# Kernel tuning notes

Hardware: AMD Instinct MI355X
Metric: run time of the kernel (lower is better)

## Reference

```python
import jax, jax.numpy as jnp
import numpy as np

IOU_THRESHOLD = 0.7


def _pairwise_iou(boxes):
    # boxes: [N, 4] as (y1, x1, y2, x2). Returns [N, N] IoU matrix.
    y1, x1, y2, x2 = boxes[:, 0], boxes[:, 1], boxes[:, 2], boxes[:, 3]
    area = (y2 - y1) * (x2 - x1)  # [N]
    iy1 = jnp.maximum(y1[:, None], y1[None, :])
    ix1 = jnp.maximum(x1[:, None], x1[None, :])
    iy2 = jnp.minimum(y2[:, None], y2[None, :])
    ix2 = jnp.minimum(x2[:, None], x2[None, :])
    ih = jnp.clip(iy2 - iy1, 0.0)
    iw = jnp.clip(ix2 - ix1, 0.0)
    inter = ih * iw
    union = area[:, None] + area[None, :] - inter
    return inter / jnp.maximum(union, 1e-9)


def setup_inputs() -> dict:
    key = jax.random.key(0)
    k1, k2, k3 = jax.random.split(key, 3)
    n = 8192
    img = 1024.0
    # Valid boxes: top-left corner + positive width/height, clipped to image.
    tl = jax.random.uniform(k1, (n, 2), dtype=jnp.float32) * (img - 64.0)
    wh = 16.0 + jax.random.uniform(k2, (n, 2), dtype=jnp.float32) * 192.0
    br = jnp.minimum(tl + wh, img)
    bounding_box = jnp.concatenate([tl, br], axis=1)  # (y1, x1, y2, x2)
    cls_score = jax.random.uniform(k3, (n,), dtype=jnp.float32)
    return {"bounding_box": bounding_box, "cls_score": cls_score}


def reference(bounding_box, cls_score):
    # Sort by score descending.
    idx = jnp.argsort(-cls_score)
    bbox = bounding_box[idx]  # [N, 4]
    # NOTE: the original module suppresses box j if ANY earlier box i (i < j)
    # in score order overlaps it (even if box i was itself suppressed), so
    # there is no sequential dependence and it vectorizes exactly:
    iou = _pairwise_iou(bbox)  # [N, N]
    suppress = jnp.triu(iou > IOU_THRESHOLD, k=1)  # row i suppresses col j, i<j
    keep = ~jnp.any(suppress, axis=0)  # [N] bool
    # Original returns bbox[keep] (dynamic shape); for jit-compatibility we
    # return the sorted boxes with suppressed rows zeroed, plus equal math.
    return bbox * keep[:, None].astype(bbox.dtype)
```

## Files before the change

kernel.cpp:

```cpp
#include <hip/hip_runtime.h>
#include <stdint.h>

#define NBOX 8192


__global__ __launch_bounds__(256) void nms_rank_kernel(
    const float4* __restrict__ bbox, const float* __restrict__ score,
    float4* __restrict__ sbox, uint32_t* __restrict__ flags)
{
    __shared__ uint64_t keys[NBOX];
    const int t = threadIdx.x;
    if (blockIdx.x == 0) flags[t] = 0;

    #pragma unroll
    for (int s = 0; s < NBOX / 256; ++s) {
        int i = t + s * 256;
        uint32_t b = __float_as_uint(score[i]);
        keys[i] = ((uint64_t)(b ^ 0xFFFFFFFFu) << 32) | (uint32_t)i;
    }
    __syncthreads();

    const int e = blockIdx.x * 16 + (t >> 4);
    const int p = t & 15;
    const uint64_t myk = keys[e];
    int cnt = 0;
    #pragma unroll 8
    for (int s = 0; s < NBOX / 16; ++s)
        cnt += (keys[s * 16 + p] < myk) ? 1 : 0;

    cnt += __shfl_down(cnt, 8, 16);
    cnt += __shfl_down(cnt, 4, 16);
    cnt += __shfl_down(cnt, 2, 16);
    cnt += __shfl_down(cnt, 1, 16);

    if (p == 0) sbox[cnt] = bbox[e];
}

__global__ __launch_bounds__(256) void nms_suppress_kernel(
    const float4* __restrict__ sbox, uint32_t* __restrict__ flags)
{
    const int w    = (int)(threadIdx.x >> 6);
    const int lane = (int)(threadIdx.x & 63);
    const int is   = (int)(blockIdx.x >> 8);
    const int jg   = ((int)(blockIdx.x & 255)) * 4 + w;
    const int j0   = jg * 8;
    const int s0   = is * 512;
    if (s0 >= j0 + 7) return;

    int nfull = (j0 - s0) >> 6;
    if (nfull < 0) nfull = 0;
    if (nfull > 8) nfull = 8;
    const int pc = nfull;
    const bool partial = (pc < 8) && (s0 + pc * 64 < j0 + 7);

    float jy1[8], jx1[8], jy2[8], jx2[8], ja[8];
    #pragma unroll
    for (int k = 0; k < 8; ++k) {
        float4 b = sbox[j0 + k];
        jy1[k] = b.x; jx1[k] = b.y; jy2[k] = b.z; jx2[k] = b.w;
        ja[k] = (b.z - b.x) * (b.w - b.y);
    }

    uint32_t hit = 0;
    float4 cur = sbox[s0 + lane];

    for (int c = 0; c < nfull; ++c) {
        float4 nxt = sbox[s0 + (c + 1) * 64 + lane];

        const float iy1 = cur.x, ix1 = cur.y, iy2 = cur.z, ix2 = cur.w;
        const float ia = (iy2 - iy1) * (ix2 - ix1);
        #pragma unroll
        for (int k = 0; k < 8; ++k) {
            float ty1 = fmaxf(iy1, jy1[k]);
            float tx1 = fmaxf(ix1, jx1[k]);
            float ty2 = fminf(iy2, jy2[k]);
            float tx2 = fminf(ix2, jx2[k]);
            float ih = fmaxf(ty2 - ty1, 0.0f);
            float iw = fmaxf(tx2 - tx1, 0.0f);
            float inter = ih * iw;
            float s = ia + ja[k];
            if (inter > 0.4110f * s) {
                float un = s - inter;
                float iou = inter / fmaxf(un, 1e-9f);
                if (iou > 0.7f) hit |= (1u << k);
            }
        }
        cur = nxt;
    }

    if (partial) {
        const int i = s0 + pc * 64 + lane;
        const float iy1 = cur.x, ix1 = cur.y, iy2 = cur.z, ix2 = cur.w;
        const float ia = (iy2 - iy1) * (ix2 - ix1);
        #pragma unroll
        for (int k = 0; k < 8; ++k) {
            float ty1 = fmaxf(iy1, jy1[k]);
            float tx1 = fmaxf(ix1, jx1[k]);
            float ty2 = fminf(iy2, jy2[k]);
            float tx2 = fminf(ix2, jx2[k]);
            float ih = fmaxf(ty2 - ty1, 0.0f);
            float iw = fmaxf(tx2 - tx1, 0.0f);
            float inter = ih * iw;
            float s = ia + ja[k];
            if ((i < j0 + k) & (inter > 0.4110f * s)) {
                float un = s - inter;
                float iou = inter / fmaxf(un, 1e-9f);
                if (iou > 0.7f) hit |= (1u << k);
            }
        }
    }

    uint32_t byte = 0;
    #pragma unroll
    for (int k = 0; k < 8; ++k)
        if (__any(hit & (1u << k))) byte |= (1u << k);
    if (lane == 0 && byte)
        atomicOr(&flags[jg >> 2], byte << ((jg & 3) * 8));
}

__global__ __launch_bounds__(256) void nms_write_kernel(
    const float4* __restrict__ sbox, const uint32_t* __restrict__ flags,
    float4* __restrict__ out)
{
    int j = blockIdx.x * 256 + threadIdx.x;
    bool sup = (flags[j >> 5] >> (j & 31)) & 1u;
    float4 v = sbox[j];
    if (sup) { v.x = 0.0f; v.y = 0.0f; v.z = 0.0f; v.w = 0.0f; }
    out[j] = v;
}

extern "C" void kernel_launch(void* const* d_in, const int* in_sizes, int n_in,
                              void* d_out, int out_size, void* d_ws, size_t ws_size,
                              hipStream_t stream) {
    const float4* bbox  = (const float4*)d_in[0];
    const float*  score = (const float*)d_in[1];
    float4* out = (float4*)d_out;
    float4* sbox = (float4*)d_ws;
    uint32_t* flags = (uint32_t*)((float*)d_ws + 4 * NBOX);

    hipLaunchKernelGGL(nms_rank_kernel, dim3(NBOX / 16), dim3(256), 0, stream,
                       bbox, score, sbox, flags);
    hipLaunchKernelGGL(nms_suppress_kernel, dim3(4096), dim3(256), 0, stream,
                       sbox, flags);
    hipLaunchKernelGGL(nms_write_kernel, dim3(NBOX / 256), dim3(256), 0, stream,
                       sbox, flags, out);
}
```

Before: 36.41 us.

## Rework rank keys to 32-bit and tile suppression over triangular block pairs

The rank kernel now keeps raw 32-bit score bits in shared memory and counts with vectorized uint4 reads plus an explicit index tie-break, replacing the 64-bit packed keys. The suppression kernel is restructured into a triangular grid. Each block stages 128 earlier boxes in shared memory and gives each thread one candidate box, which removes the wave-wide __any reductions and the redundant per-thread area recomputation. The IoU test is now a division-free double-precision comparison, and mask checks run only on diagonal tiles. The risks are that float rounding and tie-breaking on the threshold may differ slightly from the reference, and the double compares can be slower on some paths.

```diff
diff --git a/kernel.cpp b/kernel.cpp
--- a/kernel.cpp
+++ b/kernel.cpp
@@ -5,29 +5,31 @@
 
 
 __global__ __launch_bounds__(256) void nms_rank_kernel(
-    const float4* __restrict__ bbox, const float* __restrict__ score,
+    const float4* __restrict__ bbox, const uint32_t* __restrict__ scoreBits,
     float4* __restrict__ sbox, uint32_t* __restrict__ flags)
 {
-    __shared__ uint64_t keys[NBOX];
+    __shared__ uint32_t keys[NBOX];
     const int t = threadIdx.x;
     if (blockIdx.x == 0) flags[t] = 0;
 
     #pragma unroll
-    for (int s = 0; s < NBOX / 256; ++s) {
-        int i = t + s * 256;
-        uint32_t b = __float_as_uint(score[i]);
-        keys[i] = ((uint64_t)(b ^ 0xFFFFFFFFu) << 32) | (uint32_t)i;
-    }
+    for (int s = 0; s < 8; ++s)
+        ((uint4*)keys)[t + s * 256] = ((const uint4*)scoreBits)[t + s * 256];
     __syncthreads();
 
     const int e = blockIdx.x * 16 + (t >> 4);
     const int p = t & 15;
-    const uint64_t myk = keys[e];
+    const uint32_t m = keys[e];
     int cnt = 0;
-    #pragma unroll 8
-    for (int s = 0; s < NBOX / 16; ++s)
-        cnt += (keys[s * 16 + p] < myk) ? 1 : 0;
-
+    #pragma unroll 4
+    for (int s = 0; s < 128; ++s) {
+        uint4 kb = ((const uint4*)keys)[s * 16 + p];
+        int ib = s * 64 + p * 4;
+        cnt += (int)(kb.x > m) + (int)((kb.x == m) & (ib + 0 < e));
+        cnt += (int)(kb.y > m) + (int)((kb.y == m) & (ib + 1 < e));
+        cnt += (int)(kb.z > m) + (int)((kb.z == m) & (ib + 2 < e));
+        cnt += (int)(kb.w > m) + (int)((kb.w == m) & (ib + 3 < e));
+    }
     cnt += __shfl_down(cnt, 8, 16);
     cnt += __shfl_down(cnt, 4, 16);
     cnt += __shfl_down(cnt, 2, 16);
@@ -36,86 +38,61 @@
     if (p == 0) sbox[cnt] = bbox[e];
 }
 
-__global__ __launch_bounds__(256) void nms_suppress_kernel(
+__device__ __forceinline__ bool iou_hit(float4 bi, float ia,
+                                        float jy1, float jx1, float jy2,
+                                        float jx2, float ja) {
+    const double MD = (double)0.7f + 0x1.0p-25;
+    float ty1 = fmaxf(bi.x, jy1);
+    float tx1 = fmaxf(bi.y, jx1);
+    float ty2 = fminf(bi.z, jy2);
+    float tx2 = fminf(bi.w, jx2);
+    float ih = fmaxf(__fsub_rn(ty2, ty1), 0.0f);
+    float iw = fmaxf(__fsub_rn(tx2, tx1), 0.0f);
+    float inter = __fmul_rn(ih, iw);
+    float s  = __fadd_rn(ia, ja);
+    float un = __fsub_rn(s, inter);
+    return (double)inter >= MD * (double)un;
+}
+
+__global__ __launch_bounds__(256, 4) void nms_suppress_kernel(
     const float4* __restrict__ sbox, uint32_t* __restrict__ flags)
 {
-    const int w    = (int)(threadIdx.x >> 6);
-    const int lane = (int)(threadIdx.x & 63);
-    const int is   = (int)(blockIdx.x >> 8);
-    const int jg   = ((int)(blockIdx.x & 255)) * 4 + w;
-    const int j0   = jg * 8;
-    const int s0   = is * 512;
-    if (s0 >= j0 + 7) return;
+    __shared__ float4 LB[128];
+    __shared__ float  LA[128];
+    const int tid = threadIdx.x;
+    const int b = (int)blockIdx.x;
 
-    int nfull = (j0 - s0) >> 6;
-    if (nfull < 0) nfull = 0;
-    if (nfull > 8) nfull = 8;
-    const int pc = nfull;
-    const bool partial = (pc < 8) && (s0 + pc * 64 < j0 + 7);
+    int jb = (int)((sqrtf(4.0f * (float)b + 1.0f) - 1.0f) * 0.5f);
+    while ((jb + 1) * (jb + 2) <= b) ++jb;
+    while (jb * (jb + 1) > b) --jb;
+    const int t = b - jb * (jb + 1);
+    const int ibase = t * 128;
+    const int j = jb * 256 + tid;
 
-    float jy1[8], jx1[8], jy2[8], jx2[8], ja[8];
-    #pragma unroll
-    for (int k = 0; k < 8; ++k) {
-        float4 b = sbox[j0 + k];
-        jy1[k] = b.x; jx1[k] = b.y; jy2[k] = b.z; jx2[k] = b.w;
-        ja[k] = (b.z - b.x) * (b.w - b.y);
+    if (tid < 128) {
+        float4 bx = sbox[ibase + tid];
+        LB[tid] = bx;
+        LA[tid] = __fmul_rn(__fsub_rn(bx.z, bx.x), __fsub_rn(bx.w, bx.y));
     }
+    float4 bj = sbox[j];
+    const float jy1 = bj.x, jx1 = bj.y, jy2 = bj.z, jx2 = bj.w;
+    const float ja = __fmul_rn(__fsub_rn(bj.z, bj.x), __fsub_rn(bj.w, bj.y));
+    __syncthreads();
 
-    uint32_t hit = 0;
-    float4 cur = sbox[s0 + lane];
-
-    for (int c = 0; c < nfull; ++c) {
-        float4 nxt = sbox[s0 + (c + 1) * 64 + lane];
-
-        const float iy1 = cur.x, ix1 = cur.y, iy2 = cur.z, ix2 = cur.w;
-        const float ia = (iy2 - iy1) * (ix2 - ix1);
-        #pragma unroll
-        for (int k = 0; k < 8; ++k) {
-            float ty1 = fmaxf(iy1, jy1[k]);
-            float tx1 = fmaxf(ix1, jx1[k]);
-            float ty2 = fminf(iy2, jy2[k]);
-            float tx2 = fminf(ix2, jx2[k]);
-            float ih = fmaxf(ty2 - ty1, 0.0f);
-            float iw = fmaxf(tx2 - tx1, 0.0f);
-            float inter = ih * iw;
-            float s = ia + ja[k];
-            if (inter > 0.4110f * s) {
-                float un = s - inter;
-                float iou = inter / fmaxf(un, 1e-9f);
-                if (iou > 0.7f) hit |= (1u << k);
-            }
-        }
-        cur = nxt;
-    }
-
-    if (partial) {
-        const int i = s0 + pc * 64 + lane;
-        const float iy1 = cur.x, ix1 = cur.y, iy2 = cur.z, ix2 = cur.w;
-        const float ia = (iy2 - iy1) * (ix2 - ix1);
-        #pragma unroll
-        for (int k = 0; k < 8; ++k) {
-            float ty1 = fmaxf(iy1, jy1[k]);
-            float tx1 = fmaxf(ix1, jx1[k]);
-            float ty2 = fminf(iy2, jy2[k]);
-            float tx2 = fminf(ix2, jx2[k]);
-            float ih = fmaxf(ty2 - ty1, 0.0f);
-            float iw = fmaxf(tx2 - tx1, 0.0f);
-            float inter = ih * iw;
-            float s = ia + ja[k];
-            if ((i < j0 + k) & (inter > 0.4110f * s)) {
-                float un = s - inter;
-                float iou = inter / fmaxf(un, 1e-9f);
-                if (iou > 0.7f) hit |= (1u << k);
-            }
+    bool supp = false;
+    if (t < 2 * jb) {
+        #pragma unroll 4
+        for (int ii = 0; ii < 128; ++ii)
+            supp |= iou_hit(LB[ii], LA[ii], jy1, jx1, jy2, jx2, ja);
+    } else {
+        #pragma unroll 4
+        for (int ii = 0; ii < 128; ++ii) {
+            bool ok = (ibase + ii) < j;
+            supp |= ok & iou_hit(LB[ii], LA[ii], jy1, jx1, jy2, jx2, ja);
         }
     }
 
-    uint32_t byte = 0;
-    #pragma unroll
-    for (int k = 0; k < 8; ++k)
-        if (__any(hit & (1u << k))) byte |= (1u << k);
-    if (lane == 0 && byte)
-        atomicOr(&flags[jg >> 2], byte << ((jg & 3) * 8));
+    if (supp) atomicOr(&flags[j >> 5], 1u << (j & 31));
 }
 
 __global__ __launch_bounds__(256) void nms_write_kernel(
@@ -132,15 +109,15 @@
 extern "C" void kernel_launch(void* const* d_in, const int* in_sizes, int n_in,
                               void* d_out, int out_size, void* d_ws, size_t ws_size,
                               hipStream_t stream) {
-    const float4* bbox  = (const float4*)d_in[0];
-    const float*  score = (const float*)d_in[1];
+    const float4*   bbox  = (const float4*)d_in[0];
+    const uint32_t* sbits = (const uint32_t*)d_in[1];
     float4* out = (float4*)d_out;
     float4* sbox = (float4*)d_ws;
-    uint32_t* flags = (uint32_t*)((float*)d_ws + 4 * NBOX);
+    uint32_t* flags = (uint32_t*)((char*)d_ws + NBOX * 16);
 
     hipLaunchKernelGGL(nms_rank_kernel, dim3(NBOX / 16), dim3(256), 0, stream,
-                       bbox, score, sbox, flags);
-    hipLaunchKernelGGL(nms_suppress_kernel, dim3(4096), dim3(256), 0, stream,
+                       bbox, sbits, sbox, flags);
+    hipLaunchKernelGGL(nms_suppress_kernel, dim3(1056), dim3(256), 0, stream,
                        sbox, flags);
     hipLaunchKernelGGL(nms_write_kernel, dim3(NBOX / 256), dim3(256), 0, stream,
                        sbox, flags, out);
```

Result: slower. 45.16 us (+24.0%).
